# Kernel tuning notes

Hardware: AMD Instinct MI355X
Metric: run time of the kernel (lower is better)

Reference implementation:

```python
import jax, jax.numpy as jnp
import numpy as np

N, E, D, L, G = 50000, 800000, 96, 3, 256
CD, CH, LAT = 7, 5, 64
BN_EPS = 1e-5


def setup_inputs() -> dict:
    key = jax.random.key(0)
    ks = iter(jax.random.split(key, 32))
    nrm = lambda shape, s=0.1: jax.random.normal(next(ks), shape, dtype=jnp.float32) * s
    return {
        "x": jax.random.normal(next(ks), (N, D), dtype=jnp.float32),
        "cond": jax.random.normal(next(ks), (G, CD), dtype=jnp.float32),
        "edge_index": jax.random.randint(next(ks), (2, E), 0, N),
        "batch": jnp.sort(jax.random.randint(next(ks), (N,), 0, G)),
        "conv_W1": nrm((L, D, D)),
        "conv_b1": nrm((L, D)),
        "conv_g": jnp.ones((L, D), jnp.float32),
        "conv_beta": jnp.zeros((L, D), jnp.float32),
        "conv_mean": jnp.zeros((L, D), jnp.float32),
        "conv_var": jnp.ones((L, D), jnp.float32),
        "conv_W2": nrm((L, D, D)),
        "conv_b2": nrm((L, D)),
        "cW1": nrm((CD, CH)),
        "cb1": nrm((CH,)),
        "cg": jnp.ones((CH,), jnp.float32),
        "cbeta": jnp.zeros((CH,), jnp.float32),
        "cmean": jnp.zeros((CH,), jnp.float32),
        "cvar": jnp.ones((CH,), jnp.float32),
        "cW2": nrm((CH, CH)),
        "cb2": nrm((CH,)),
        "bn_g": jnp.ones((D + CH,), jnp.float32),
        "bn_b": jnp.zeros((D + CH,), jnp.float32),
        "bn_mean": jnp.zeros((D + CH,), jnp.float32),
        "bn_var": jnp.ones((D + CH,), jnp.float32),
        "fc_W": nrm((D + CH, LAT)),
        "fc_b": nrm((LAT,)),
    }


def _bn(h, g, b, mu, var):
    # BatchNorm1d in eval mode: normalize with running stats
    return (h - mu) * (g / jnp.sqrt(var + BN_EPS)) + b


def reference(x, cond, edge_index, batch,
              conv_W1, conv_b1, conv_g, conv_beta, conv_mean, conv_var, conv_W2, conv_b2,
              cW1, cb1, cg, cbeta, cmean, cvar, cW2, cb2,
              bn_g, bn_b, bn_mean, bn_var, fc_W, fc_b):
    src, dst = edge_index[0], edge_index[1]
    n_nodes = x.shape[0]
    h = x
    for l in range(conv_W1.shape[0]):
        # GINConv (eps=0): h_i <- MLP(h_i + sum_{j in N(i)} h_j)
        agg = jax.ops.segment_sum(h[src], dst, num_segments=n_nodes)  # [N, D]
        h = h + agg
        h = jax.nn.leaky_relu(h @ conv_W1[l] + conv_b1[l], 0.2)
        h = _bn(h, conv_g[l], conv_beta[l], conv_mean[l], conv_var[l])
        h = jax.nn.leaky_relu(h @ conv_W2[l] + conv_b2[l], 0.2)
        # dropout is identity in eval mode
    pooled = jax.ops.segment_sum(h, batch, num_segments=cond.shape[0])  # [G, D]
    # conditioning MLP: Linear -> BN -> ReLU -> Linear -> ReLU
    c = cond @ cW1 + cb1
    c = jax.nn.relu(_bn(c, cg, cbeta, cmean, cvar))
    c = jax.nn.relu(c @ cW2 + cb2)
    out = jnp.concatenate([c, pooled], axis=1)  # [G, CH + D]
    out = _bn(out, bn_g, bn_b, bn_mean, bn_var)
    return out @ fc_W + fc_b  # [G, LAT]
```

## Files before the change

### kernel.cpp

```cpp
#include <hip/hip_runtime.h>

#define BN_EPS 1e-5f

__device__ __forceinline__ float lrelu(float x){ return x > 0.f ? x : 0.2f*x; }

struct F3 { float x, y, z; };


__global__ __launch_bounds__(256) void hist_k(const int* __restrict__ dst,
                                              int* __restrict__ deg, int E){
  int e = blockIdx.x*256 + threadIdx.x;
  if (e < E) atomicAdd(&deg[dst[e]], 1);
}

__global__ __launch_bounds__(256) void scan1_k(int* __restrict__ degoff,
                                               int* __restrict__ bsum, int N){
  __shared__ int s[256];
  int t = threadIdx.x, i = blockIdx.x*256 + t;
  int v = (i < N) ? degoff[i] : 0;
  s[t] = v; __syncthreads();
  int x = v;
  for (int d = 1; d < 256; d <<= 1){
    int y = (t >= d) ? s[t-d] : 0;
    __syncthreads();
    x += y; s[t] = x;
    __syncthreads();
  }
  if (i < N) degoff[i] = x - v;
  if (t == 255) bsum[blockIdx.x] = x;
}

__global__ __launch_bounds__(256) void scan2_k(int* __restrict__ bsum, int nb){
  __shared__ int s[256];
  int t = threadIdx.x;
  int v = (t < nb) ? bsum[t] : 0;
  s[t] = v; __syncthreads();
  int x = v;
  for (int d = 1; d < 256; d <<= 1){
    int y = (t >= d) ? s[t-d] : 0;
    __syncthreads();
    x += y; s[t] = x;
    __syncthreads();
  }
  if (t < nb) bsum[t] = x - v;
}

__global__ __launch_bounds__(256) void scan3_k(int* __restrict__ off,
                                               const int* __restrict__ bsum,
                                               int N, int E){
  int i = blockIdx.x*256 + threadIdx.x;
  if (i < N) off[i] += bsum[blockIdx.x];
  if (i == 0) off[N] = E;
}

#define EB 4096

__global__ __launch_bounds__(256) void bhist_k(const int* __restrict__ dst,
                                               int* __restrict__ bcnt, int E){
  __shared__ int bh[512];
  int t = threadIdx.x;
  bh[t] = 0; bh[t+256] = 0;
  __syncthreads();
  int e0 = blockIdx.x*EB;
  for (int i = 0; i < EB/256; ++i){
    int e = e0 + i*256 + t;
    if (e < E) atomicAdd(&bh[dst[e] >> 7], 1);
  }
  __syncthreads();
  if (bh[t])     atomicAdd(&bcnt[t],     bh[t]);
  if (bh[t+256]) atomicAdd(&bcnt[t+256], bh[t+256]);
}

__global__ __launch_bounds__(512) void bscan_k(const int* __restrict__ bcnt,
                                               int* __restrict__ bkt_off,
                                               int* __restrict__ gcur, int E){
  __shared__ int s[512];
  int t = threadIdx.x;
  int v = bcnt[t];
  s[t] = v; __syncthreads();
  int x = v;
  for (int d = 1; d < 512; d <<= 1){
    int y = (t >= d) ? s[t-d] : 0;
    __syncthreads();
    x += y; s[t] = x;
    __syncthreads();
  }
  bkt_off[t] = x - v;
  gcur[t]    = x - v;
  if (t == 511) bkt_off[512] = E;
}

__global__ __launch_bounds__(256) void bpart_k(const int* __restrict__ src,
                                               const int* __restrict__ dst,
                                               int* __restrict__ gcur,
                                               int2* __restrict__ ebuf, int E){
  __shared__ int bh[512];
  __shared__ int base[512];
  int t = threadIdx.x;
  bh[t] = 0; bh[t+256] = 0;
  __syncthreads();
  int e0 = blockIdx.x*EB;
  for (int i = 0; i < EB/256; ++i){
    int e = e0 + i*256 + t;
    if (e < E) atomicAdd(&bh[dst[e] >> 7], 1);
  }
  __syncthreads();
  #pragma unroll
  for (int h = 0; h < 2; ++h){
    int b = t + h*256;
    base[b] = bh[b] ? atomicAdd(&gcur[b], bh[b]) : 0;
  }
  __syncthreads();
  for (int i = 0; i < EB/256; ++i){
    int e = e0 + i*256 + t;
    if (e < E){
      int s = src[e], d = dst[e];
      int p = atomicAdd(&base[d >> 7], 1);
      ebuf[p] = make_int2(s, d);
    }
  }
}

__global__ __launch_bounds__(256) void bscat_k(const int2* __restrict__ ebuf,
                                               const int* __restrict__ bkt_off,
                                               const int* __restrict__ off,
                                               int* __restrict__ srcs, int N){
  __shared__ int lcur[128];
  int b = blockIdx.x, t = threadIdx.x;
  int node_lo = b << 7;
  if (t < 128){
    int n = node_lo + t;
    lcur[t] = (n < N) ? off[n] : 0;
  }
  __syncthreads();
  int eb = bkt_off[b], ee = bkt_off[b+1];
  for (int e = eb + t; e < ee; e += 256){
    int2 sd = ebuf[e];
    int p = atomicAdd(&lcur[sd.y - node_lo], 1);
    srcs[p] = sd.x;
  }
}

__global__ __launch_bounds__(256) void agg_k(const float* __restrict__ hin,
                                             float* __restrict__ hout,
                                             const int* __restrict__ off,
                                             const int* __restrict__ srcs, int N){
  int node = blockIdx.x*8 + (threadIdx.x >> 5);
  int ln = threadIdx.x & 31;
  if (node >= N) return;
  F3 a = *((const F3*)(hin + (size_t)node*96) + ln);
  float bx = 0.f, by = 0.f, bz = 0.f;
  int jb = off[node], je = off[node+1];
  int j = jb;
  for (; j+1 < je; j += 2){
    int s0 = srcs[j], s1 = srcs[j+1];
    F3 q0 = *((const F3*)(hin + (size_t)s0*96) + ln);
    F3 q1 = *((const F3*)(hin + (size_t)s1*96) + ln);
    a.x += q0.x; a.y += q0.y; a.z += q0.z;
    bx  += q1.x; by  += q1.y; bz  += q1.z;
  }
  if (j < je){
    int s0 = srcs[j];
    F3 q0 = *((const F3*)(hin + (size_t)s0*96) + ln);
    a.x += q0.x; a.y += q0.y; a.z += q0.z;
  }
  a.x += bx; a.y += by; a.z += bz;
  *((F3*)(hout + (size_t)node*96) + ln) = a;
}

__global__ __launch_bounds__(512) void mlp_sw_k(
    const float* __restrict__ hin, float* __restrict__ hout,
    const float* __restrict__ W1, const float* __restrict__ b1,
    const float* __restrict__ g, const float* __restrict__ beta,
    const float* __restrict__ mean, const float* __restrict__ var,
    const float* __restrict__ W2, const float* __restrict__ b2, int N)
{
  __shared__ float hT[96*67];
  int t = threadIdx.x;
  int nbase = blockIdx.x * 64;
  int lim = (N - nbase) * 96;
  const float* hbase = hin + (size_t)nbase*96;

  #pragma unroll
  for (int i = 0; i < 12; ++i){
    int tid = t + 512*i;
    float v = (tid < lim) ? hbase[tid] : 0.f;
    int n = tid / 96, k = tid - n*96;
    hT[k*67 + n] = v;
  }
  __syncthreads();

  int ln = t & 63;
  int d0 = __builtin_amdgcn_readfirstlane((t >> 6) * 12);

  float acc[12];
  #pragma unroll
  for (int j = 0; j < 12; ++j) acc[j] = b1[d0+j];
  for (int kc = 0; kc < 96; kc += 8){
    float hc[8];
    #pragma unroll
    for (int i = 0; i < 8; ++i) hc[i] = hT[(kc+i)*67 + ln];
    #pragma unroll
    for (int i = 0; i < 8; ++i){
      const float* wr = W1 + (kc+i)*96 + d0;
      #pragma unroll
      for (int j = 0; j < 12; ++j) acc[j] = fmaf(hc[i], wr[j], acc[j]);
    }
  }
  __syncthreads();

  #pragma unroll
  for (int j = 0; j < 12; ++j){
    int d = d0 + j;
    float s = g[d] * rsqrtf(var[d] + BN_EPS);
    float m = lrelu(acc[j]);
    hT[d*67 + ln] = (m - mean[d])*s + beta[d];
  }
  __syncthreads();

  #pragma unroll
  for (int j = 0; j < 12; ++j) acc[j] = b2[d0+j];
  for (int kc = 0; kc < 96; kc += 8){
    float hc[8];
    #pragma unroll
    for (int i = 0; i < 8; ++i) hc[i] = hT[(kc+i)*67 + ln];
    #pragma unroll
    for (int i = 0; i < 8; ++i){
      const float* wr = W2 + (kc+i)*96 + d0;
      #pragma unroll
      for (int j = 0; j < 12; ++j) acc[j] = fmaf(hc[i], wr[j], acc[j]);
    }
  }
  __syncthreads();

  #pragma unroll
  for (int j = 0; j < 12; ++j)
    hT[(d0+j)*67 + ln] = lrelu(acc[j]);
  __syncthreads();

  float* obase = hout + (size_t)nbase*96;
  #pragma unroll
  for (int i = 0; i < 12; ++i){
    int tid = t + 512*i;
    int n = tid / 96, k = tid - n*96;
    if (tid < lim) obase[tid] = hT[k*67 + n];
  }
}


__global__ __launch_bounds__(256) void bounds_k(const int* __restrict__ batch,
                                                int* __restrict__ go, int N, int G){
  int i = blockIdx.x*256 + threadIdx.x;
  if (i >= N) return;
  int b = batch[i];
  int prev = (i == 0) ? -1 : batch[i-1];
  for (int g = prev+1; g <= b; ++g) go[g] = i;
  if (i == N-1){
    for (int g = b+1; g <= G; ++g) go[g] = N;
  }
}

__global__ __launch_bounds__(384) void poolfinal_k(
    const float* __restrict__ h, const int* __restrict__ go,
    const float* __restrict__ cond,
    const float* __restrict__ cW1, const float* __restrict__ cb1,
    const float* __restrict__ cg, const float* __restrict__ cbeta,
    const float* __restrict__ cmean, const float* __restrict__ cvar,
    const float* __restrict__ cW2, const float* __restrict__ cb2,
    const float* __restrict__ bn_g, const float* __restrict__ bn_b,
    const float* __restrict__ bn_mean, const float* __restrict__ bn_var,
    const float* __restrict__ fcW, const float* __restrict__ fcb,
    float* __restrict__ out)
{
  __shared__ float ps[4][96];
  __shared__ float pl[96];
  int g = blockIdx.x, t = threadIdx.x;
  int s = t / 96, d = t - s*96;
  {
    float acc = 0.f;
    int nb = go[g], ne = go[g+1];
    for (int n = nb + s; n < ne; n += 4) acc += h[(size_t)n*96 + d];
    ps[s][d] = acc;
  }
  __syncthreads();
  if (t < 96) pl[t] = ps[0][t] + ps[1][t] + ps[2][t] + ps[3][t];
  __syncthreads();

  if (t < 64){
    float cin[7];
    #pragma unroll
    for (int j = 0; j < 7; ++j) cin[j] = cond[g*7+j];
    float c1[5];
    #pragma unroll
    for (int i = 0; i < 5; ++i){
      float a = cb1[i];
      #pragma unroll
      for (int j = 0; j < 7; ++j) a = fmaf(cin[j], cW1[j*5+i], a);
      float sc = cg[i] * rsqrtf(cvar[i] + BN_EPS);
      a = (a - cmean[i])*sc + cbeta[i];
      c1[i] = a > 0.f ? a : 0.f;
    }
    float c2[5];
    #pragma unroll
    for (int i = 0; i < 5; ++i){
      float a = cb2[i];
      #pragma unroll
      for (int j = 0; j < 5; ++j) a = fmaf(c1[j], cW2[j*5+i], a);
      c2[i] = a > 0.f ? a : 0.f;
    }
    float acc = fcb[t];
    #pragma unroll
    for (int j = 0; j < 5; ++j){
      float sc = bn_g[j] * rsqrtf(bn_var[j] + BN_EPS);
      float nb = (c2[j] - bn_mean[j])*sc + bn_b[j];
      acc = fmaf(nb, fcW[j*64 + t], acc);
    }
    for (int j = 5; j < 101; ++j){
      float vj = pl[j-5];
      float sc = bn_g[j] * rsqrtf(bn_var[j] + BN_EPS);
      float nb = (vj - bn_mean[j])*sc + bn_b[j];
      acc = fmaf(nb, fcW[j*64 + t], acc);
    }
    out[g*64 + t] = acc;
  }
}


extern "C" void kernel_launch(void* const* d_in, const int* in_sizes, int n_in,
                              void* d_out, int out_size, void* d_ws, size_t ws_size,
                              hipStream_t stream)
{
  const float* x         = (const float*)d_in[0];
  const float* cond      = (const float*)d_in[1];
  const int*   ei        = (const int*)  d_in[2];
  const int*   batch     = (const int*)  d_in[3];
  const float* conv_W1   = (const float*)d_in[4];
  const float* conv_b1   = (const float*)d_in[5];
  const float* conv_g    = (const float*)d_in[6];
  const float* conv_beta = (const float*)d_in[7];
  const float* conv_mean = (const float*)d_in[8];
  const float* conv_var  = (const float*)d_in[9];
  const float* conv_W2   = (const float*)d_in[10];
  const float* conv_b2   = (const float*)d_in[11];
  const float* cW1       = (const float*)d_in[12];
  const float* cb1       = (const float*)d_in[13];
  const float* cg        = (const float*)d_in[14];
  const float* cbeta     = (const float*)d_in[15];
  const float* cmean     = (const float*)d_in[16];
  const float* cvar      = (const float*)d_in[17];
  const float* cW2       = (const float*)d_in[18];
  const float* cb2       = (const float*)d_in[19];
  const float* bn_g      = (const float*)d_in[20];
  const float* bn_b      = (const float*)d_in[21];
  const float* bn_mean   = (const float*)d_in[22];
  const float* bn_var    = (const float*)d_in[23];
  const float* fc_W      = (const float*)d_in[24];
  const float* fc_b      = (const float*)d_in[25];

  const int D = 96;
  int N = in_sizes[0] / D;
  int G = in_sizes[1] / 7;
  int E = in_sizes[2] / 2;
  const int* src = ei;
  const int* dst = ei + E;

  char* p = (char*)d_ws;
  auto carve = [&](size_t bytes)->void*{
    void* r = (void*)p; p += (bytes + 255) & ~(size_t)255; return r;
  };
  int*   off     = (int*)  carve((size_t)(N+1)*4);
  int*   bsum    = (int*)  carve(256*4);
  int*   bcnt    = (int*)  carve(512*4);
  int*   bkt_off = (int*)  carve(513*4);
  int*   gcur    = (int*)  carve(512*4);
  int2*  ebuf    = (int2*) carve((size_t)E*8);
  int*   srcs    = (int*)  carve((size_t)E*4);
  int*   go      = (int*)  carve((size_t)(G+1)*4);
  float* hA      = (float*)carve((size_t)N*D*4);
  float* hB      = (float*)carve((size_t)N*D*4);

  int gE = (E+255)/256, gN = (N+255)/256, gEB = (E+EB-1)/EB;

  hipMemsetAsync(off,  0, (size_t)(N+1)*4, stream);
  hipMemsetAsync(bcnt, 0, 512*4, stream);
  hist_k <<<gE, 256, 0, stream>>>(dst, off, E);
  scan1_k<<<gN, 256, 0, stream>>>(off, bsum, N);
  scan2_k<<<1,  256, 0, stream>>>(bsum, gN);
  scan3_k<<<gN, 256, 0, stream>>>(off, bsum, N, E);
  bhist_k<<<gEB, 256, 0, stream>>>(dst, bcnt, E);
  bscan_k<<<1,  512, 0, stream>>>(bcnt, bkt_off, gcur, E);
  bpart_k<<<gEB, 256, 0, stream>>>(src, dst, gcur, ebuf, E);
  bscat_k<<<512, 256, 0, stream>>>(ebuf, bkt_off, off, srcs, N);
  bounds_k<<<gN, 256, 0, stream>>>(batch, go, N, G);

  const float* hin = x;
  int nblk = (N+63)/64;
  for (int l = 0; l < 3; ++l){
    agg_k<<<(N+7)/8, 256, 0, stream>>>(hin, hB, off, srcs, N);
    mlp_sw_k<<<nblk, 512, 0, stream>>>(hB, hA,
        conv_W1 + (size_t)l*D*D, conv_b1 + l*D,
        conv_g + l*D, conv_beta + l*D, conv_mean + l*D, conv_var + l*D,
        conv_W2 + (size_t)l*D*D, conv_b2 + l*D, N);
    hin = hA;
  }

  poolfinal_k<<<G, 384, 0, stream>>>(hA, go, cond,
                                     cW1, cb1, cg, cbeta, cmean, cvar,
                                     cW2, cb2, bn_g, bn_b, bn_mean, bn_var,
                                     fc_W, fc_b, (float*)d_out);
}
```

Baseline: 490.6 us.

## Register-tile node MLP with LDS-staged weights and fuse degree/bucket histograms

Replaces the 512-thread MLP kernel with a 128-thread version. Each thread computes a 4-node by 12-feature register tile, and the 96x96 weight matrices are staged in LDS instead of being read from global memory per FMA. The second layer writes directly to global memory with float4 stores, which drops the transpose back through LDS. The degree histogram and bucket histogram passes are merged into one kernel so the dst array is read once. The cost is higher register pressure (48 accumulators) and more LDS per block, which may lower occupancy.

After: 558.9 us. +13.9%, slower.

```diff
diff --git a/kernel.cpp b/kernel.cpp
--- a/kernel.cpp
+++ b/kernel.cpp
@@ -6,11 +6,27 @@
 
 struct F3 { float x, y, z; };
 
-
-__global__ __launch_bounds__(256) void hist_k(const int* __restrict__ dst,
-                                              int* __restrict__ deg, int E){
-  int e = blockIdx.x*256 + threadIdx.x;
-  if (e < E) atomicAdd(&deg[dst[e]], 1);
+#define EB 4096
+
+__global__ __launch_bounds__(256) void hist2_k(const int* __restrict__ dst,
+                                               int* __restrict__ deg,
+                                               int* __restrict__ bcnt, int E){
+  __shared__ int bh[512];
+  int t = threadIdx.x;
+  bh[t] = 0; bh[t+256] = 0;
+  __syncthreads();
+  int e0 = blockIdx.x*EB;
+  for (int i = 0; i < EB/256; ++i){
+    int e = e0 + i*256 + t;
+    if (e < E){
+      int d = dst[e];
+      atomicAdd(&deg[d], 1);
+      atomicAdd(&bh[d >> 7], 1);
+    }
+  }
+  __syncthreads();
+  if (bh[t])     atomicAdd(&bcnt[t],     bh[t]);
+  if (bh[t+256]) atomicAdd(&bcnt[t+256], bh[t+256]);
 }
 
 __global__ __launch_bounds__(256) void scan1_k(int* __restrict__ degoff,
@@ -51,24 +67,6 @@
   int i = blockIdx.x*256 + threadIdx.x;
   if (i < N) off[i] += bsum[blockIdx.x];
   if (i == 0) off[N] = E;
-}
-
-#define EB 4096
-
-__global__ __launch_bounds__(256) void bhist_k(const int* __restrict__ dst,
-                                               int* __restrict__ bcnt, int E){
-  __shared__ int bh[512];
-  int t = threadIdx.x;
-  bh[t] = 0; bh[t+256] = 0;
-  __syncthreads();
-  int e0 = blockIdx.x*EB;
-  for (int i = 0; i < EB/256; ++i){
-    int e = e0 + i*256 + t;
-    if (e < E) atomicAdd(&bh[dst[e] >> 7], 1);
-  }
-  __syncthreads();
-  if (bh[t])     atomicAdd(&bcnt[t],     bh[t]);
-  if (bh[t+256]) atomicAdd(&bcnt[t+256], bh[t+256]);
 }
 
 __global__ __launch_bounds__(512) void bscan_k(const int* __restrict__ bcnt,
@@ -168,85 +166,118 @@
   *((F3*)(hout + (size_t)node*96) + ln) = a;
 }
 
-__global__ __launch_bounds__(512) void mlp_sw_k(
+__global__ __launch_bounds__(128) void mlp_mt_k(
     const float* __restrict__ hin, float* __restrict__ hout,
     const float* __restrict__ W1, const float* __restrict__ b1,
     const float* __restrict__ g, const float* __restrict__ beta,
     const float* __restrict__ mean, const float* __restrict__ var,
     const float* __restrict__ W2, const float* __restrict__ b2, int N)
 {
-  __shared__ float hT[96*67];
+  __shared__ float Ws[96*96];
+  __shared__ float hT[96*68];
   int t = threadIdx.x;
   int nbase = blockIdx.x * 64;
   int lim = (N - nbase) * 96;
   const float* hbase = hin + (size_t)nbase*96;
 
   #pragma unroll
-  for (int i = 0; i < 12; ++i){
-    int tid = t + 512*i;
-    float v = (tid < lim) ? hbase[tid] : 0.f;
-    int n = tid / 96, k = tid - n*96;
-    hT[k*67 + n] = v;
-  }
-  __syncthreads();
-
-  int ln = t & 63;
-  int d0 = __builtin_amdgcn_readfirstlane((t >> 6) * 12);
-
-  float acc[12];
-  #pragma unroll
-  for (int j = 0; j < 12; ++j) acc[j] = b1[d0+j];
-  for (int kc = 0; kc < 96; kc += 8){
-    float hc[8];
-    #pragma unroll
-    for (int i = 0; i < 8; ++i) hc[i] = hT[(kc+i)*67 + ln];
-    #pragma unroll
-    for (int i = 0; i < 8; ++i){
-      const float* wr = W1 + (kc+i)*96 + d0;
-      #pragma unroll
-      for (int j = 0; j < 12; ++j) acc[j] = fmaf(hc[i], wr[j], acc[j]);
-    }
-  }
-  __syncthreads();
-
+  for (int i = 0; i < 18; ++i)
+    ((float4*)Ws)[t + 128*i] = ((const float4*)W1)[t + 128*i];
+  #pragma unroll
+  for (int i = 0; i < 48; ++i){
+    int e = t + 128*i;
+    float v = (e < lim) ? hbase[e] : 0.f;
+    int n = e / 96, k = e - n*96;
+    hT[k*68 + n] = v;
+  }
+  __syncthreads();
+
+  int dg = t & 7, np = t >> 3;
+  int d0 = dg*12, n0 = np*4;
+
+  float acc[48];
+  #pragma unroll
+  for (int j = 0; j < 12; ++j){
+    float bj = b1[d0+j];
+    #pragma unroll
+    for (int i = 0; i < 4; ++i) acc[j*4+i] = bj;
+  }
+  #pragma unroll 2
+  for (int k = 0; k < 96; ++k){
+    float4 hv = *(const float4*)&hT[k*68 + n0];
+    const float* wr = &Ws[k*96 + d0];
+    float w[12];
+    *(float4*)&w[0] = *(const float4*)(wr);
+    *(float4*)&w[4] = *(const float4*)(wr+4);
+    *(float4*)&w[8] = *(const float4*)(wr+8);
+    #pragma unroll
+    for (int j = 0; j < 12; ++j){
+      acc[j*4+0] = fmaf(hv.x, w[j], acc[j*4+0]);
+      acc[j*4+1] = fmaf(hv.y, w[j], acc[j*4+1]);
+      acc[j*4+2] = fmaf(hv.z, w[j], acc[j*4+2]);
+      acc[j*4+3] = fmaf(hv.w, w[j], acc[j*4+3]);
+    }
+  }
+  __syncthreads();
+
+  #pragma unroll
+  for (int i = 0; i < 18; ++i)
+    ((float4*)Ws)[t + 128*i] = ((const float4*)W2)[t + 128*i];
   #pragma unroll
   for (int j = 0; j < 12; ++j){
     int d = d0 + j;
     float s = g[d] * rsqrtf(var[d] + BN_EPS);
-    float m = lrelu(acc[j]);
-    hT[d*67 + ln] = (m - mean[d])*s + beta[d];
-  }
-  __syncthreads();
-
-  #pragma unroll
-  for (int j = 0; j < 12; ++j) acc[j] = b2[d0+j];
-  for (int kc = 0; kc < 96; kc += 8){
-    float hc[8];
-    #pragma unroll
-    for (int i = 0; i < 8; ++i) hc[i] = hT[(kc+i)*67 + ln];
-    #pragma unroll
-    for (int i = 0; i < 8; ++i){
-      const float* wr = W2 + (kc+i)*96 + d0;
-      #pragma unroll
-      for (int j = 0; j < 12; ++j) acc[j] = fmaf(hc[i], wr[j], acc[j]);
-    }
-  }
-  __syncthreads();
-
-  #pragma unroll
-  for (int j = 0; j < 12; ++j)
-    hT[(d0+j)*67 + ln] = lrelu(acc[j]);
-  __syncthreads();
-
-  float* obase = hout + (size_t)nbase*96;
-  #pragma unroll
-  for (int i = 0; i < 12; ++i){
-    int tid = t + 512*i;
-    int n = tid / 96, k = tid - n*96;
-    if (tid < lim) obase[tid] = hT[k*67 + n];
-  }
-}
-
+    float mu = mean[d], bt = beta[d];
+    float4 m;
+    m.x = (lrelu(acc[j*4+0]) - mu)*s + bt;
+    m.y = (lrelu(acc[j*4+1]) - mu)*s + bt;
+    m.z = (lrelu(acc[j*4+2]) - mu)*s + bt;
+    m.w = (lrelu(acc[j*4+3]) - mu)*s + bt;
+    *(float4*)&hT[d*68 + n0] = m;
+  }
+  __syncthreads();
+
+  #pragma unroll
+  for (int j = 0; j < 12; ++j){
+    float bj = b2[d0+j];
+    #pragma unroll
+    for (int i = 0; i < 4; ++i) acc[j*4+i] = bj;
+  }
+  #pragma unroll 2
+  for (int k = 0; k < 96; ++k){
+    float4 hv = *(const float4*)&hT[k*68 + n0];
+    const float* wr = &Ws[k*96 + d0];
+    float w[12];
+    *(float4*)&w[0] = *(const float4*)(wr);
+    *(float4*)&w[4] = *(const float4*)(wr+4);
+    *(float4*)&w[8] = *(const float4*)(wr+8);
+    #pragma unroll
+    for (int j = 0; j < 12; ++j){
+      acc[j*4+0] = fmaf(hv.x, w[j], acc[j*4+0]);
+      acc[j*4+1] = fmaf(hv.y, w[j], acc[j*4+1]);
+      acc[j*4+2] = fmaf(hv.z, w[j], acc[j*4+2]);
+      acc[j*4+3] = fmaf(hv.w, w[j], acc[j*4+3]);
+    }
+  }
+
+  #pragma unroll
+  for (int i = 0; i < 4; ++i){
+    int node = nbase + n0 + i;
+    if (node < N){
+      float* op = hout + (size_t)node*96 + d0;
+      float4 o;
+      o.x = lrelu(acc[0*4+i]);  o.y = lrelu(acc[1*4+i]);
+      o.z = lrelu(acc[2*4+i]);  o.w = lrelu(acc[3*4+i]);
+      *(float4*)(op) = o;
+      o.x = lrelu(acc[4*4+i]);  o.y = lrelu(acc[5*4+i]);
+      o.z = lrelu(acc[6*4+i]);  o.w = lrelu(acc[7*4+i]);
+      *(float4*)(op+4) = o;
+      o.x = lrelu(acc[8*4+i]);  o.y = lrelu(acc[9*4+i]);
+      o.z = lrelu(acc[10*4+i]); o.w = lrelu(acc[11*4+i]);
+      *(float4*)(op+8) = o;
+    }
+  }
+}
 
 __global__ __launch_bounds__(256) void bounds_k(const int* __restrict__ batch,
                                                 int* __restrict__ go, int N, int G){
@@ -379,15 +410,14 @@
   float* hA      = (float*)carve((size_t)N*D*4);
   float* hB      = (float*)carve((size_t)N*D*4);
 
-  int gE = (E+255)/256, gN = (N+255)/256, gEB = (E+EB-1)/EB;
+  int gN = (N+255)/256, gEB = (E+EB-1)/EB;
 
   hipMemsetAsync(off,  0, (size_t)(N+1)*4, stream);
   hipMemsetAsync(bcnt, 0, 512*4, stream);
-  hist_k <<<gE, 256, 0, stream>>>(dst, off, E);
+  hist2_k<<<gEB, 256, 0, stream>>>(dst, off, bcnt, E);
   scan1_k<<<gN, 256, 0, stream>>>(off, bsum, N);
   scan2_k<<<1,  256, 0, stream>>>(bsum, gN);
   scan3_k<<<gN, 256, 0, stream>>>(off, bsum, N, E);
-  bhist_k<<<gEB, 256, 0, stream>>>(dst, bcnt, E);
   bscan_k<<<1,  512, 0, stream>>>(bcnt, bkt_off, gcur, E);
   bpart_k<<<gEB, 256, 0, stream>>>(src, dst, gcur, ebuf, E);
   bscat_k<<<512, 256, 0, stream>>>(ebuf, bkt_off, off, srcs, N);
@@ -397,7 +427,7 @@
   int nblk = (N+63)/64;
   for (int l = 0; l < 3; ++l){
     agg_k<<<(N+7)/8, 256, 0, stream>>>(hin, hB, off, srcs, N);
-    mlp_sw_k<<<nblk, 512, 0, stream>>>(hB, hA,
+    mlp_mt_k<<<nblk, 128, 0, stream>>>(hB, hA,
         conv_W1 + (size_t)l*D*D, conv_b1 + l*D,
         conv_g + l*D, conv_beta + l*D, conv_mean + l*D, conv_var + l*D,
         conv_W2 + (size_t)l*D*D, conv_b2 + l*D, N);
```

## Run GIN MLP layers on bf16x3 MFMA and fuse degree histograms

Applied to the files above, without the earlier changes.

The per-layer MLP moves from scalar FMA to matrix-core MFMA (16x16x32 bf16). To keep near-fp32 accuracy it splits activations and weights into hi/lo bf16 parts and sums three products. A new prep kernel packs the weights once per call into the MFMA operand layout. The per-node degree histogram and the bucket histogram are also merged into one pass over dst, which drops one kernel launch and one read of the edge array. The costs are three MFMAs per tile, a small rounding difference from fp32, and an extra weight-packing kernel.

Result: faster. 427.8 us (-12.8%).

```diff
diff --git a/kernel.cpp b/kernel.cpp
--- a/kernel.cpp
+++ b/kernel.cpp
@@ -6,11 +6,30 @@
 
 struct F3 { float x, y, z; };
 
-
-__global__ __launch_bounds__(256) void hist_k(const int* __restrict__ dst,
-                                              int* __restrict__ deg, int E){
-  int e = blockIdx.x*256 + threadIdx.x;
-  if (e < E) atomicAdd(&deg[dst[e]], 1);
+typedef __attribute__((ext_vector_type(8))) short short8v;
+typedef __attribute__((ext_vector_type(4))) float f32x4;
+
+#define EB 4096
+
+__global__ __launch_bounds__(256) void hist2_k(const int* __restrict__ dst,
+                                               int* __restrict__ deg,
+                                               int* __restrict__ bcnt, int E){
+  __shared__ int bh[512];
+  int t = threadIdx.x;
+  bh[t] = 0; bh[t+256] = 0;
+  __syncthreads();
+  int e0 = blockIdx.x*EB;
+  for (int i = 0; i < EB/256; ++i){
+    int e = e0 + i*256 + t;
+    if (e < E){
+      int d = dst[e];
+      atomicAdd(&deg[d], 1);
+      atomicAdd(&bh[d >> 7], 1);
+    }
+  }
+  __syncthreads();
+  if (bh[t])     atomicAdd(&bcnt[t],     bh[t]);
+  if (bh[t+256]) atomicAdd(&bcnt[t+256], bh[t+256]);
 }
 
 __global__ __launch_bounds__(256) void scan1_k(int* __restrict__ degoff,
@@ -51,24 +70,6 @@
   int i = blockIdx.x*256 + threadIdx.x;
   if (i < N) off[i] += bsum[blockIdx.x];
   if (i == 0) off[N] = E;
-}
-
-#define EB 4096
-
-__global__ __launch_bounds__(256) void bhist_k(const int* __restrict__ dst,
-                                               int* __restrict__ bcnt, int E){
-  __shared__ int bh[512];
-  int t = threadIdx.x;
-  bh[t] = 0; bh[t+256] = 0;
-  __syncthreads();
-  int e0 = blockIdx.x*EB;
-  for (int i = 0; i < EB/256; ++i){
-    int e = e0 + i*256 + t;
-    if (e < E) atomicAdd(&bh[dst[e] >> 7], 1);
-  }
-  __syncthreads();
-  if (bh[t])     atomicAdd(&bcnt[t],     bh[t]);
-  if (bh[t+256]) atomicAdd(&bcnt[t+256], bh[t+256]);
 }
 
 __global__ __launch_bounds__(512) void bscan_k(const int* __restrict__ bcnt,
@@ -168,85 +169,158 @@
   *((F3*)(hout + (size_t)node*96) + ln) = a;
 }
 
-__global__ __launch_bounds__(512) void mlp_sw_k(
+__global__ __launch_bounds__(256) void wprep_k(const float* __restrict__ W1b,
+                                               const float* __restrict__ W2b,
+                                               short* __restrict__ Wpk){
+  int mat = blockIdx.x;
+  int layer = mat >> 1, which = mat & 1;
+  const float* src = (which ? W2b : W1b) + (size_t)layer*9216;
+  short* hi = Wpk + (size_t)mat*18432;
+  short* lo = hi + 9216;
+  for (int i = threadIdx.x; i < 9216; i += 256){
+    int j = i & 7, lane = (i >> 3) & 63, grp = i >> 9;
+    int kb = grp / 6, nt = grp - 6*kb;
+    int k = 32*kb + 8*(lane>>4) + j;
+    int n = 16*nt + (lane&15);
+    float v = src[k*96 + n];
+    unsigned b = __float_as_uint(v);
+    unsigned short hb = (unsigned short)(b >> 16);
+    float hf = __uint_as_float((unsigned)hb << 16);
+    float lof = v - hf;
+    hi[i] = (short)hb;
+    lo[i] = (short)(__float_as_uint(lof) >> 16);
+  }
+}
+
+__global__ __launch_bounds__(256) void mlp_mfma_k(
     const float* __restrict__ hin, float* __restrict__ hout,
-    const float* __restrict__ W1, const float* __restrict__ b1,
-    const float* __restrict__ g, const float* __restrict__ beta,
-    const float* __restrict__ mean, const float* __restrict__ var,
-    const float* __restrict__ W2, const float* __restrict__ b2, int N)
+    const short* __restrict__ Whi1, const short* __restrict__ Wlo1,
+    const short* __restrict__ Whi2, const short* __restrict__ Wlo2,
+    const float* __restrict__ b1, const float* __restrict__ g,
+    const float* __restrict__ beta, const float* __restrict__ mean,
+    const float* __restrict__ var, const float* __restrict__ b2, int N)
 {
-  __shared__ float hT[96*67];
+  __shared__ float hT[64*97];
   int t = threadIdx.x;
   int nbase = blockIdx.x * 64;
   int lim = (N - nbase) * 96;
   const float* hbase = hin + (size_t)nbase*96;
 
   #pragma unroll
-  for (int i = 0; i < 12; ++i){
-    int tid = t + 512*i;
+  for (int i = 0; i < 24; ++i){
+    int tid = t + 256*i;
     float v = (tid < lim) ? hbase[tid] : 0.f;
     int n = tid / 96, k = tid - n*96;
-    hT[k*67 + n] = v;
-  }
-  __syncthreads();
-
-  int ln = t & 63;
-  int d0 = __builtin_amdgcn_readfirstlane((t >> 6) * 12);
-
-  float acc[12];
-  #pragma unroll
-  for (int j = 0; j < 12; ++j) acc[j] = b1[d0+j];
-  for (int kc = 0; kc < 96; kc += 8){
-    float hc[8];
-    #pragma unroll
-    for (int i = 0; i < 8; ++i) hc[i] = hT[(kc+i)*67 + ln];
-    #pragma unroll
-    for (int i = 0; i < 8; ++i){
-      const float* wr = W1 + (kc+i)*96 + d0;
-      #pragma unroll
-      for (int j = 0; j < 12; ++j) acc[j] = fmaf(hc[i], wr[j], acc[j]);
-    }
-  }
-  __syncthreads();
-
-  #pragma unroll
-  for (int j = 0; j < 12; ++j){
-    int d = d0 + j;
-    float s = g[d] * rsqrtf(var[d] + BN_EPS);
-    float m = lrelu(acc[j]);
-    hT[d*67 + ln] = (m - mean[d])*s + beta[d];
-  }
-  __syncthreads();
-
-  #pragma unroll
-  for (int j = 0; j < 12; ++j) acc[j] = b2[d0+j];
-  for (int kc = 0; kc < 96; kc += 8){
-    float hc[8];
-    #pragma unroll
-    for (int i = 0; i < 8; ++i) hc[i] = hT[(kc+i)*67 + ln];
-    #pragma unroll
-    for (int i = 0; i < 8; ++i){
-      const float* wr = W2 + (kc+i)*96 + d0;
-      #pragma unroll
-      for (int j = 0; j < 12; ++j) acc[j] = fmaf(hc[i], wr[j], acc[j]);
-    }
-  }
-  __syncthreads();
-
-  #pragma unroll
-  for (int j = 0; j < 12; ++j)
-    hT[(d0+j)*67 + ln] = lrelu(acc[j]);
+    hT[n*97 + k] = v;
+  }
+  __syncthreads();
+
+  int l = t & 63, w = t >> 6;
+  int kgrp = l >> 4;
+  int arow = 16*w + (l & 15);
+  int col  = l & 15;
+
+  short8v ah[3], al[3];
+  #pragma unroll
+  for (int kb = 0; kb < 3; ++kb){
+    const float* ap = &hT[arow*97 + 32*kb + 8*kgrp];
+    #pragma unroll
+    for (int j = 0; j < 8; ++j){
+      float v = ap[j];
+      unsigned bits = __float_as_uint(v);
+      unsigned short hb = (unsigned short)(bits >> 16);
+      float hf = __uint_as_float((unsigned)hb << 16);
+      unsigned short lb = (unsigned short)(__float_as_uint(v - hf) >> 16);
+      ah[kb][j] = (short)hb;
+      al[kb][j] = (short)lb;
+    }
+  }
+
+  float mid[6][4];
+  {
+    const short8v* BH = (const short8v*)Whi1;
+    const short8v* BL = (const short8v*)Wlo1;
+    #pragma unroll
+    for (int nt = 0; nt < 6; ++nt){
+      int d = 16*nt + col;
+      float bv = b1[d];
+      f32x4 acc; acc[0]=bv; acc[1]=bv; acc[2]=bv; acc[3]=bv;
+      #pragma unroll
+      for (int kb = 0; kb < 3; ++kb){
+        short8v bh = BH[(kb*6 + nt)*64 + l];
+        short8v bl = BL[(kb*6 + nt)*64 + l];
+        acc = __builtin_amdgcn_mfma_f32_16x16x32_bf16(ah[kb], bh, acc, 0,0,0);
+        acc = __builtin_amdgcn_mfma_f32_16x16x32_bf16(ah[kb], bl, acc, 0,0,0);
+        acc = __builtin_amdgcn_mfma_f32_16x16x32_bf16(al[kb], bh, acc, 0,0,0);
+      }
+      float s  = g[d] * rsqrtf(var[d] + BN_EPS);
+      float mu = mean[d], bt = beta[d];
+      #pragma unroll
+      for (int r = 0; r < 4; ++r)
+        mid[nt][r] = (lrelu(acc[r]) - mu)*s + bt;
+    }
+  }
+  __syncthreads();
+
+  #pragma unroll
+  for (int nt = 0; nt < 6; ++nt)
+    #pragma unroll
+    for (int r = 0; r < 4; ++r)
+      hT[(16*w + 4*kgrp + r)*97 + 16*nt + col] = mid[nt][r];
+  __syncthreads();
+
+  #pragma unroll
+  for (int kb = 0; kb < 3; ++kb){
+    const float* ap = &hT[arow*97 + 32*kb + 8*kgrp];
+    #pragma unroll
+    for (int j = 0; j < 8; ++j){
+      float v = ap[j];
+      unsigned bits = __float_as_uint(v);
+      unsigned short hb = (unsigned short)(bits >> 16);
+      float hf = __uint_as_float((unsigned)hb << 16);
+      unsigned short lb = (unsigned short)(__float_as_uint(v - hf) >> 16);
+      ah[kb][j] = (short)hb;
+      al[kb][j] = (short)lb;
+    }
+  }
+
+  float outr[6][4];
+  {
+    const short8v* BH = (const short8v*)Whi2;
+    const short8v* BL = (const short8v*)Wlo2;
+    #pragma unroll
+    for (int nt = 0; nt < 6; ++nt){
+      float bv = b2[16*nt + col];
+      f32x4 acc; acc[0]=bv; acc[1]=bv; acc[2]=bv; acc[3]=bv;
+      #pragma unroll
+      for (int kb = 0; kb < 3; ++kb){
+        short8v bh = BH[(kb*6 + nt)*64 + l];
+        short8v bl = BL[(kb*6 + nt)*64 + l];
+        acc = __builtin_amdgcn_mfma_f32_16x16x32_bf16(ah[kb], bh, acc, 0,0,0);
+        acc = __builtin_amdgcn_mfma_f32_16x16x32_bf16(ah[kb], bl, acc, 0,0,0);
+        acc = __builtin_amdgcn_mfma_f32_16x16x32_bf16(al[kb], bh, acc, 0,0,0);
+      }
+      #pragma unroll
+      for (int r = 0; r < 4; ++r) outr[nt][r] = lrelu(acc[r]);
+    }
+  }
+  __syncthreads();
+
+  #pragma unroll
+  for (int nt = 0; nt < 6; ++nt)
+    #pragma unroll
+    for (int r = 0; r < 4; ++r)
+      hT[(16*w + 4*kgrp + r)*97 + 16*nt + col] = outr[nt][r];
   __syncthreads();
 
   float* obase = hout + (size_t)nbase*96;
   #pragma unroll
-  for (int i = 0; i < 12; ++i){
-    int tid = t + 512*i;
+  for (int i = 0; i < 24; ++i){
+    int tid = t + 256*i;
     int n = tid / 96, k = tid - n*96;
-    if (tid < lim) obase[tid] = hT[k*67 + n];
-  }
-}
-
+    if (tid < lim) obase[tid] = hT[n*97 + k];
+  }
+}
 
 __global__ __launch_bounds__(256) void bounds_k(const int* __restrict__ batch,
                                                 int* __restrict__ go, int N, int G){
@@ -376,18 +450,19 @@
   int2*  ebuf    = (int2*) carve((size_t)E*8);
   int*   srcs    = (int*)  carve((size_t)E*4);
   int*   go      = (int*)  carve((size_t)(G+1)*4);
+  short* Wpk     = (short*)carve(6*18432*2);
   float* hA      = (float*)carve((size_t)N*D*4);
   float* hB      = (float*)carve((size_t)N*D*4);
 
-  int gE = (E+255)/256, gN = (N+255)/256, gEB = (E+EB-1)/EB;
+  int gN = (N+255)/256, gEB = (E+EB-1)/EB;
 
   hipMemsetAsync(off,  0, (size_t)(N+1)*4, stream);
   hipMemsetAsync(bcnt, 0, 512*4, stream);
-  hist_k <<<gE, 256, 0, stream>>>(dst, off, E);
+  wprep_k<<<6, 256, 0, stream>>>(conv_W1, conv_W2, Wpk);
+  hist2_k<<<gEB, 256, 0, stream>>>(dst, off, bcnt, E);
   scan1_k<<<gN, 256, 0, stream>>>(off, bsum, N);
   scan2_k<<<1,  256, 0, stream>>>(bsum, gN);
   scan3_k<<<gN, 256, 0, stream>>>(off, bsum, N, E);
-  bhist_k<<<gEB, 256, 0, stream>>>(dst, bcnt, E);
   bscan_k<<<1,  512, 0, stream>>>(bcnt, bkt_off, gcur, E);
   bpart_k<<<gEB, 256, 0, stream>>>(src, dst, gcur, ebuf, E);
   bscat_k<<<512, 256, 0, stream>>>(ebuf, bkt_off, off, srcs, N);
@@ -397,10 +472,13 @@
   int nblk = (N+63)/64;
   for (int l = 0; l < 3; ++l){
     agg_k<<<(N+7)/8, 256, 0, stream>>>(hin, hB, off, srcs, N);
-    mlp_sw_k<<<nblk, 512, 0, stream>>>(hB, hA,
-        conv_W1 + (size_t)l*D*D, conv_b1 + l*D,
-        conv_g + l*D, conv_beta + l*D, conv_mean + l*D, conv_var + l*D,
-        conv_W2 + (size_t)l*D*D, conv_b2 + l*D, N);
+    const short* Whi1 = Wpk + (size_t)(2*l)  *18432;
+    const short* Wlo1 = Whi1 + 9216;
+    const short* Whi2 = Wpk + (size_t)(2*l+1)*18432;
+    const short* Wlo2 = Whi2 + 9216;
+    mlp_mfma_k<<<nblk, 256, 0, stream>>>(hB, hA, Whi1, Wlo1, Whi2, Wlo2,
+        conv_b1 + l*D, conv_g + l*D, conv_beta + l*D, conv_mean + l*D,
+        conv_var + l*D, conv_b2 + l*D, N);
     hin = hA;
   }
 
```
